# Kernel optimization log

Hardware: AMD Instinct MI355X
Metric: run time of the kernel (lower is better)

## Reference

```python
import jax, jax.numpy as jnp
import numpy as np

N_NODES = 10000
N_EDGES = 640000
D_IN, D_HID, D_OUT = 128, 256, 64


def setup_inputs() -> dict:
    key = jax.random.key(0)
    k = jax.random.split(key, 8)
    h = jax.random.normal(k[0], (N_NODES, D_IN), dtype=jnp.float32)
    w = jax.random.uniform(k[1], (N_EDGES, 1), dtype=jnp.float32)
    src = jax.random.randint(k[2], (N_EDGES,), 0, N_NODES, dtype=jnp.int32)
    dst = jax.random.randint(k[3], (N_EDGES,), 0, N_NODES, dtype=jnp.int32)
    W1 = jax.random.normal(k[4], (2 * D_IN, D_HID), dtype=jnp.float32) * (1.0 / np.sqrt(2 * D_IN))
    b1 = jnp.zeros((D_HID,), dtype=jnp.float32)
    W2 = jax.random.normal(k[5], (2 * D_HID, D_OUT), dtype=jnp.float32) * (1.0 / np.sqrt(2 * D_HID))
    b2 = jnp.zeros((D_OUT,), dtype=jnp.float32)
    return {"h": h, "w": w, "src": src, "dst": dst, "W1": W1, "b1": b1, "W2": W2, "b2": b2}


def _sage_layer(h, w, src, dst, W, b, n_nodes):
    # message: m_e = h[src_e] * w_e  (scalar edge weight broadcast over features)
    m = h[src] * w  # [E, D]
    # mean scatter-reduce over incoming edges per destination node
    s = jax.ops.segment_sum(m, dst, num_segments=n_nodes)          # [N, D]
    deg = jax.ops.segment_sum(jnp.ones((dst.shape[0],), h.dtype), dst, num_segments=n_nodes)
    h_N = jnp.where(deg[:, None] > 0, s / jnp.maximum(deg, 1.0)[:, None], 0.0)
    # concat + linear
    return jnp.concatenate([h, h_N], axis=1) @ W + b


def reference(h, w, src, dst, W1, b1, W2, b2):
    n = h.shape[0]
    x = _sage_layer(h, w, src, dst, W1, b1, n)
    x = jax.nn.relu(x)
    return _sage_layer(x, w, src, dst, W2, b2, n)
```

## Files before the change

kernel.cpp:

```cpp
#include <hip/hip_runtime.h>
#include <hip/hip_fp16.h>


#define NSUB 4
#define CAPS 64

typedef _Float16 f16x8 __attribute__((ext_vector_type(8)));
typedef float f32x4 __attribute__((ext_vector_type(4)));


__global__ __launch_bounds__(256) void prep_k(const float* __restrict__ h,
                                              const float* __restrict__ W1,
                                              const float* __restrict__ W2,
                                              int* __restrict__ cursor,
                                              __half* __restrict__ hh,
                                              __half* __restrict__ W1z,
                                              __half* __restrict__ W2z,
                                              int NC, int NH4) {
  const int t = blockIdx.x * blockDim.x + threadIdx.x;
  if (t < NC) {
    cursor[t] = 0;
    return;
  }
  const int tc = t - NC;
  if (tc < NH4) {
    const float4 v = reinterpret_cast<const float4*>(h)[tc];
    reinterpret_cast<__half2*>(hh)[2 * tc] = __floats2half2_rn(v.x, v.y);
    reinterpret_cast<__half2*>(hh)[2 * tc + 1] = __floats2half2_rn(v.z, v.w);
    return;
  }
  const int tw1 = tc - NH4;
  if (tw1 < 8192) {
    const int ln = tw1 & 63;
    const int nt = (tw1 >> 6) & 15;
    const int kc = tw1 >> 10;
    const int kbase = kc * 32 + (ln >> 4) * 8;
    const int n = nt * 16 + (ln & 15);
    __half tmp[8];
#pragma unroll
    for (int j = 0; j < 8; ++j)
      tmp[j] = __float2half_rn(W1[(size_t)(kbase + j) * 256 + n]);
    *reinterpret_cast<uint4*>(W1z + (size_t)tw1 * 8) = *reinterpret_cast<uint4*>(tmp);
    return;
  }
  const int tw2 = tw1 - 8192;
  if (tw2 < 4096) {
    const int ln = tw2 & 63;
    const int nt = (tw2 >> 6) & 7;
    const int kc = tw2 >> 9;
    const int kbase = kc * 32 + (ln >> 4) * 8;
    const int np = nt * 16 + (ln & 15);
    __half tmp[8];
#pragma unroll
    for (int j = 0; j < 8; ++j) {
      const int k = kbase + j;
      const float v = (np < 64) ? W2[(size_t)k * 64 + np]
                                : W2[(size_t)(256 + k) * 64 + (np - 64)];
      tmp[j] = __float2half_rn(v);
    }
    *reinterpret_cast<uint4*>(W2z + (size_t)tw2 * 8) = *reinterpret_cast<uint4*>(tmp);
  }
}


__global__ __launch_bounds__(256) void fill_k(const int* __restrict__ src,
                                              const int* __restrict__ dst,
                                              const float* __restrict__ w,
                                              int* __restrict__ cursor,
                                              unsigned int* __restrict__ ebuf,
                                              int E, int N) {
  const int grp = blockIdx.x & 7;
  const int bi = blockIdx.x >> 3;
  const int nbg = gridDim.x >> 3;
  const int chunk = (N + 7) >> 3;
  const int lo = grp * chunk;
  const int hi = min(N, lo + chunk);
  for (int i = bi * 256 + threadIdx.x; i < E; i += nbg * 256) {
    const int d = dst[i];
    if (d >= lo && d < hi) {
      const int sub = i & (NSUB - 1);
      const int p = atomicAdd(&cursor[d * NSUB + sub], 1);
      if (p < CAPS) {
        const __half hw = __float2half_rn(w[i]);
        ebuf[((size_t)(d * NSUB + sub)) * CAPS + p] =
            ((unsigned int)src[i] << 16) | (unsigned int)__half_as_ushort(hw);
      }
    }
  }
}

#define ACC8(q, wt)                                              \
  {                                                              \
    const float2 t0 = __half22float2(*(const __half2*)&(q).x);   \
    const float2 t1 = __half22float2(*(const __half2*)&(q).y);   \
    const float2 t2 = __half22float2(*(const __half2*)&(q).z);   \
    const float2 t3 = __half22float2(*(const __half2*)&(q).w);   \
    a[0] += t0.x * (wt); a[1] += t0.y * (wt);                    \
    a[2] += t1.x * (wt); a[3] += t1.y * (wt);                    \
    a[4] += t2.x * (wt); a[5] += t2.y * (wt);                    \
    a[6] += t3.x * (wt); a[7] += t3.y * (wt);                    \
  }


__global__ __launch_bounds__(256) void agg1_k(const __half* __restrict__ hh,
                                              const unsigned int* __restrict__ ebuf,
                                              const int* __restrict__ cnt,
                                              __half* __restrict__ G1, int N) {
  const int n = blockIdx.x * 4 + (threadIdx.x >> 6);
  if (n >= N) return;
  const int lane = threadIdx.x & 63;
  const int g = lane >> 4;
  const int f = lane & 15;
  const uint4* __restrict__ H = reinterpret_cast<const uint4*>(hh);
  float a[8] = {};
  int deg = 0;
#pragma unroll
  for (int seg = 0; seg < NSUB; ++seg) {
    const int m = min(cnt[n * NSUB + seg], CAPS);
    deg += m;
    const unsigned int* __restrict__ bkt = ebuf + ((size_t)(n * NSUB + seg)) * CAPS;
    const unsigned int pk = (lane < m) ? bkt[lane] : 0u;
    int j = 0;
    for (; j + 7 < m; j += 8) {
      const unsigned int pA = __shfl(pk, j + g);
      const unsigned int pB = __shfl(pk, j + 4 + g);
      const int eA = (int)(pA >> 16), eB = (int)(pB >> 16);
      const float wA = __half2float(__ushort_as_half((unsigned short)pA));
      const float wB = __half2float(__ushort_as_half((unsigned short)pB));
      const uint4 qA = H[(size_t)eA * 16 + f];
      const uint4 qB = H[(size_t)eB * 16 + f];
      ACC8(qA, wA)
      ACC8(qB, wB)
    }
    for (; j < m; j += 4) {
      const int jj = j + g;
      const unsigned int p = __shfl(pk, jj < m ? jj : (m - 1));
      float wt = __half2float(__ushort_as_half((unsigned short)p));
      if (jj >= m) wt = 0.f;
      const uint4 q = H[(size_t)(p >> 16) * 16 + f];
      ACC8(q, wt)
    }
  }
#pragma unroll
  for (int r = 0; r < 8; ++r) {
    a[r] += __shfl_xor(a[r], 16);
    a[r] += __shfl_xor(a[r], 32);
  }
  if (lane < 16) {
    const float inv = (deg > 0) ? 1.0f / (float)deg : 0.0f;
    __half tmp[8];
#pragma unroll
    for (int r = 0; r < 8; ++r) tmp[r] = __float2half_rn(a[r] * inv);
    reinterpret_cast<uint4*>(G1)[(size_t)n * 16 + f] = *reinterpret_cast<uint4*>(tmp);
  }
}


__global__ __launch_bounds__(256) void gemm1zu_k(const __half* __restrict__ hh,
                                                 const __half* __restrict__ G1,
                                                 const __half* __restrict__ W1z,
                                                 const float* __restrict__ b1,
                                                 const __half* __restrict__ W2z,
                                                 __half* __restrict__ Z,
                                                 float* __restrict__ U) {
  const int tid = threadIdx.x;
  const int w = tid >> 6, lane = tid & 63;
  const int m0 = blockIdx.x * 16;
  const int row_in = m0 + (lane & 15);
  const int qoff = (lane >> 4) * 8;
  const int colq = lane & 15;
  const int rowq = (lane >> 4) * 4;

  f32x4 acc[4] = {};
  const __half* __restrict__ Ah = hh + (size_t)row_in * 128;
  const __half* __restrict__ Ag = G1 + (size_t)row_in * 128;
#pragma unroll
  for (int kc = 0; kc < 8; ++kc) {
    const __half* asrc = (kc < 4) ? (Ah + kc * 32 + qoff) : (Ag + (kc - 4) * 32 + qoff);
    const f16x8 af = *reinterpret_cast<const f16x8*>(asrc);
    const __half* bbase = W1z + ((size_t)(kc * 16 + w * 4) * 64 + lane) * 8;
#pragma unroll
    for (int nt = 0; nt < 4; ++nt) {
      const f16x8 bf = *reinterpret_cast<const f16x8*>(bbase + (size_t)nt * 64 * 8);
      acc[nt] = __builtin_amdgcn_mfma_f32_16x16x32_f16(af, bf, acc[nt], 0, 0, 0);
    }
  }
  __shared__ alignas(16) __half Hs[16][264];
#pragma unroll
  for (int nt = 0; nt < 4; ++nt) {
    const int col = w * 64 + nt * 16 + colq;
    const float bz = b1[col];
#pragma unroll
    for (int r = 0; r < 4; ++r)
      Hs[rowq + r][col] = __float2half_rn(fmaxf(acc[nt][r] + bz, 0.f));
  }
  __syncthreads();

  f32x4 accz[2] = {};
#pragma unroll
  for (int kc = 0; kc < 8; ++kc) {
    const f16x8 af = *reinterpret_cast<const f16x8*>(&Hs[lane & 15][kc * 32 + qoff]);
    const __half* bbase = W2z + ((size_t)(kc * 8 + w * 2) * 64 + lane) * 8;
#pragma unroll
    for (int nt = 0; nt < 2; ++nt) {
      const f16x8 bf = *reinterpret_cast<const f16x8*>(bbase + (size_t)nt * 64 * 8);
      accz[nt] = __builtin_amdgcn_mfma_f32_16x16x32_f16(af, bf, accz[nt], 0, 0, 0);
    }
  }
  __shared__ float S[16][132];
#pragma unroll
  for (int nt = 0; nt < 2; ++nt) {
    const int col = w * 32 + nt * 16 + colq;
#pragma unroll
    for (int r = 0; r < 4; ++r) S[rowq + r][col] = accz[nt][r];
  }
  __syncthreads();
  {
    const int row = tid >> 4, c4 = tid & 15;
    const float4 v = make_float4(S[row][c4 * 4], S[row][c4 * 4 + 1],
                                 S[row][c4 * 4 + 2], S[row][c4 * 4 + 3]);
    *reinterpret_cast<float4*>(&U[(size_t)(m0 + row) * 64 + c4 * 4]) = v;
  }
  if (tid < 128) {
    const int row = tid >> 3, c8 = tid & 7;
    const float* s = &S[row][64 + c8 * 8];
    const __half2 h0 = __floats2half2_rn(s[0], s[1]);
    const __half2 h1 = __floats2half2_rn(s[2], s[3]);
    const __half2 h2 = __floats2half2_rn(s[4], s[5]);
    const __half2 h3 = __floats2half2_rn(s[6], s[7]);
    uint4 q;
    q.x = *reinterpret_cast<const unsigned int*>(&h0);
    q.y = *reinterpret_cast<const unsigned int*>(&h1);
    q.z = *reinterpret_cast<const unsigned int*>(&h2);
    q.w = *reinterpret_cast<const unsigned int*>(&h3);
    *reinterpret_cast<uint4*>(&Z[(size_t)(m0 + row) * 64 + c8 * 8]) = q;
  }
}


__global__ __launch_bounds__(256) void agg2z_k(const __half* __restrict__ Z,
                                               const float* __restrict__ U,
                                               const float* __restrict__ b2,
                                               const unsigned int* __restrict__ ebuf,
                                               const int* __restrict__ cnt,
                                               float* __restrict__ out, int N) {
  const int n = blockIdx.x * 4 + (threadIdx.x >> 6);
  if (n >= N) return;
  const int lane = threadIdx.x & 63;
  const int g = lane >> 3;
  const int f = lane & 7;
  const uint4* __restrict__ Zr = reinterpret_cast<const uint4*>(Z);
  float a[8] = {};
  int deg = 0;
#pragma unroll
  for (int seg = 0; seg < NSUB; ++seg) {
    const int m = min(cnt[n * NSUB + seg], CAPS);
    deg += m;
    const unsigned int* __restrict__ bkt = ebuf + ((size_t)(n * NSUB + seg)) * CAPS;
    const unsigned int pk = (lane < m) ? bkt[lane] : 0u;
    int j = 0;
    for (; j + 15 < m; j += 16) {
      const unsigned int pA = __shfl(pk, j + g);
      const unsigned int pB = __shfl(pk, j + 8 + g);
      const int eA = (int)(pA >> 16), eB = (int)(pB >> 16);
      const float wA = __half2float(__ushort_as_half((unsigned short)pA));
      const float wB = __half2float(__ushort_as_half((unsigned short)pB));
      const uint4 qA = Zr[(size_t)eA * 8 + f];
      const uint4 qB = Zr[(size_t)eB * 8 + f];
      ACC8(qA, wA)
      ACC8(qB, wB)
    }
    for (; j < m; j += 8) {
      const int jj = j + g;
      const unsigned int p = __shfl(pk, jj < m ? jj : (m - 1));
      float wt = __half2float(__ushort_as_half((unsigned short)p));
      if (jj >= m) wt = 0.f;
      const uint4 q = Zr[(size_t)(p >> 16) * 8 + f];
      ACC8(q, wt)
    }
  }
#pragma unroll
  for (int r = 0; r < 8; ++r) {
    a[r] += __shfl_xor(a[r], 8);
    a[r] += __shfl_xor(a[r], 16);
    a[r] += __shfl_xor(a[r], 32);
  }
  if (lane < 8) {
    const float inv = (deg > 0) ? 1.0f / (float)deg : 0.0f;
    const float4 u0 = *reinterpret_cast<const float4*>(&U[(size_t)n * 64 + f * 8]);
    const float4 u1 = *reinterpret_cast<const float4*>(&U[(size_t)n * 64 + f * 8 + 4]);
    const float4 z0 = *reinterpret_cast<const float4*>(&b2[f * 8]);
    const float4 z1 = *reinterpret_cast<const float4*>(&b2[f * 8 + 4]);
    float4 o0, o1;
    o0.x = a[0] * inv + u0.x + z0.x;
    o0.y = a[1] * inv + u0.y + z0.y;
    o0.z = a[2] * inv + u0.z + z0.z;
    o0.w = a[3] * inv + u0.w + z0.w;
    o1.x = a[4] * inv + u1.x + z1.x;
    o1.y = a[5] * inv + u1.y + z1.y;
    o1.z = a[6] * inv + u1.z + z1.z;
    o1.w = a[7] * inv + u1.w + z1.w;
    *reinterpret_cast<float4*>(&out[(size_t)n * 64 + f * 8]) = o0;
    *reinterpret_cast<float4*>(&out[(size_t)n * 64 + f * 8 + 4]) = o1;
  }
}


extern "C" void kernel_launch(void* const* d_in, const int* in_sizes, int n_in,
                              void* d_out, int out_size, void* d_ws, size_t ws_size,
                              hipStream_t stream) {
  const float* h   = (const float*)d_in[0];
  const float* w   = (const float*)d_in[1];
  const int*   src = (const int*)d_in[2];
  const int*   dst = (const int*)d_in[3];
  const float* W1  = (const float*)d_in[4];
  const float* b1  = (const float*)d_in[5];
  const float* W2  = (const float*)d_in[6];
  const float* b2  = (const float*)d_in[7];
  float* out = (float*)d_out;

  const int N = in_sizes[0] / 128;
  const int E = in_sizes[2];

  char* ws = (char*)d_ws;
  size_t o = 0;
  auto alloc = [&](size_t bytes) -> void* {
    void* p = ws + o;
    o = (o + bytes + 255) & ~(size_t)255;
    return p;
  };
  int*          cursor = (int*)alloc((size_t)N * NSUB * 4);
  unsigned int* ebuf   = (unsigned int*)alloc((size_t)N * NSUB * CAPS * 4);
  __half*       hh     = (__half*)alloc((size_t)N * 128 * 2);
  __half*       G1     = (__half*)alloc((size_t)N * 128 * 2);
  __half*       Z      = (__half*)alloc((size_t)N * 64 * 2);
  float*        U      = (float*)alloc((size_t)N * 64 * 4);
  __half*       W1z    = (__half*)alloc((size_t)256 * 256 * 2);
  __half*       W2z    = (__half*)alloc((size_t)256 * 128 * 2);

  const int NC = N * NSUB;
  const int NH4 = N * 32;
  const int prep_threads = NC + NH4 + 8192 + 4096;
  prep_k<<<(prep_threads + 255) / 256, 256, 0, stream>>>(h, W1, W2, cursor, hh,
                                                         W1z, W2z, NC, NH4);
  fill_k<<<2048, 256, 0, stream>>>(src, dst, w, cursor, ebuf, E, N);
  agg1_k<<<(N + 3) / 4, 256, 0, stream>>>(hh, ebuf, cursor, G1, N);
  gemm1zu_k<<<N / 16, 256, 0, stream>>>(hh, G1, W1z, b1, W2z, Z, U);
  agg2z_k<<<(N + 3) / 4, 256, 0, stream>>>(Z, U, b2, ebuf, cursor, out, N);
}
```

Baseline: 144.2 us.

## Merge prep into fill kernel, split node aggregation across two waves, remap blocks

Zeroing the cursors moves to a memset, and the h/weight fp16 conversion is folded into the fill kernel as extra blocks, which removes a launch. agg1 now splits each node's four sub-buckets across two waves and combines the partial sums through shared memory. agg1 and agg2 remap blocks so neighbouring block IDs touch the same destination-node chunk as fill_k's grouping. The intent is more parallelism per node and fewer launches, in exchange for an extra __syncthreads and shared-memory traffic.

```diff
diff --git a/kernel.cpp b/kernel.cpp
--- a/kernel.cpp
+++ b/kernel.cpp
@@ -9,27 +9,49 @@
 typedef float f32x4 __attribute__((ext_vector_type(4)));
 
 
-__global__ __launch_bounds__(256) void prep_k(const float* __restrict__ h,
+#define FB 2048
+
+__global__ __launch_bounds__(256) void fill_k(const int* __restrict__ src,
+                                              const int* __restrict__ dst,
+                                              const float* __restrict__ w,
+                                              const float* __restrict__ h,
                                               const float* __restrict__ W1,
                                               const float* __restrict__ W2,
                                               int* __restrict__ cursor,
+                                              unsigned int* __restrict__ ebuf,
                                               __half* __restrict__ hh,
                                               __half* __restrict__ W1z,
                                               __half* __restrict__ W2z,
-                                              int NC, int NH4) {
-  const int t = blockIdx.x * blockDim.x + threadIdx.x;
-  if (t < NC) {
-    cursor[t] = 0;
+                                              int E, int N, int NH4) {
+  if (blockIdx.x < FB) {
+    const int grp = blockIdx.x & 7;
+    const int bi = blockIdx.x >> 3;
+    const int nbg = FB >> 3;
+    const int chunk = (N + 7) >> 3;
+    const int lo = grp * chunk;
+    const int hi = min(N, lo + chunk);
+    for (int i = bi * 256 + threadIdx.x; i < E; i += nbg * 256) {
+      const int d = dst[i];
+      if (d >= lo && d < hi) {
+        const int sub = i & (NSUB - 1);
+        const int p = atomicAdd(&cursor[d * NSUB + sub], 1);
+        if (p < CAPS) {
+          const __half hw = __float2half_rn(w[i]);
+          ebuf[((size_t)(d * NSUB + sub)) * CAPS + p] =
+              ((unsigned int)src[i] << 16) | (unsigned int)__half_as_ushort(hw);
+        }
+      }
+    }
     return;
   }
-  const int tc = t - NC;
-  if (tc < NH4) {
-    const float4 v = reinterpret_cast<const float4*>(h)[tc];
-    reinterpret_cast<__half2*>(hh)[2 * tc] = __floats2half2_rn(v.x, v.y);
-    reinterpret_cast<__half2*>(hh)[2 * tc + 1] = __floats2half2_rn(v.z, v.w);
+  const int t = (blockIdx.x - FB) * 256 + threadIdx.x;
+  if (t < NH4) {
+    const float4 v = reinterpret_cast<const float4*>(h)[t];
+    reinterpret_cast<__half2*>(hh)[2 * t] = __floats2half2_rn(v.x, v.y);
+    reinterpret_cast<__half2*>(hh)[2 * t + 1] = __floats2half2_rn(v.z, v.w);
     return;
   }
-  const int tw1 = tc - NH4;
+  const int tw1 = t - NH4;
   if (tw1 < 8192) {
     const int ln = tw1 & 63;
     const int nt = (tw1 >> 6) & 15;
@@ -59,33 +81,6 @@
       tmp[j] = __float2half_rn(v);
     }
     *reinterpret_cast<uint4*>(W2z + (size_t)tw2 * 8) = *reinterpret_cast<uint4*>(tmp);
-  }
-}
-
-
-__global__ __launch_bounds__(256) void fill_k(const int* __restrict__ src,
-                                              const int* __restrict__ dst,
-                                              const float* __restrict__ w,
-                                              int* __restrict__ cursor,
-                                              unsigned int* __restrict__ ebuf,
-                                              int E, int N) {
-  const int grp = blockIdx.x & 7;
-  const int bi = blockIdx.x >> 3;
-  const int nbg = gridDim.x >> 3;
-  const int chunk = (N + 7) >> 3;
-  const int lo = grp * chunk;
-  const int hi = min(N, lo + chunk);
-  for (int i = bi * 256 + threadIdx.x; i < E; i += nbg * 256) {
-    const int d = dst[i];
-    if (d >= lo && d < hi) {
-      const int sub = i & (NSUB - 1);
-      const int p = atomicAdd(&cursor[d * NSUB + sub], 1);
-      if (p < CAPS) {
-        const __half hw = __float2half_rn(w[i]);
-        ebuf[((size_t)(d * NSUB + sub)) * CAPS + p] =
-            ((unsigned int)src[i] << 16) | (unsigned int)__half_as_ushort(hw);
-      }
-    }
   }
 }
 
@@ -106,39 +101,51 @@
                                               const unsigned int* __restrict__ ebuf,
                                               const int* __restrict__ cnt,
                                               __half* __restrict__ G1, int N) {
-  const int n = blockIdx.x * 4 + (threadIdx.x >> 6);
-  if (n >= N) return;
+  const int chunk = (N + 7) >> 3;
+  const int g8 = blockIdx.x & 7;
+  const int k = blockIdx.x >> 3;
+  const int wv = threadIdx.x >> 6;
+  const int node_sel = wv >> 1;
+  const int half = wv & 1;
+  const int loc = k * 2 + node_sel;
+  const int n = g8 * chunk + loc;
   const int lane = threadIdx.x & 63;
   const int g = lane >> 4;
   const int f = lane & 15;
   const uint4* __restrict__ H = reinterpret_cast<const uint4*>(hh);
+  __shared__ float part[2][2][16][8];
+  __shared__ int degs[2][2];
   float a[8] = {};
   int deg = 0;
-#pragma unroll
-  for (int seg = 0; seg < NSUB; ++seg) {
-    const int m = min(cnt[n * NSUB + seg], CAPS);
-    deg += m;
-    const unsigned int* __restrict__ bkt = ebuf + ((size_t)(n * NSUB + seg)) * CAPS;
-    const unsigned int pk = (lane < m) ? bkt[lane] : 0u;
-    int j = 0;
-    for (; j + 7 < m; j += 8) {
-      const unsigned int pA = __shfl(pk, j + g);
-      const unsigned int pB = __shfl(pk, j + 4 + g);
-      const int eA = (int)(pA >> 16), eB = (int)(pB >> 16);
-      const float wA = __half2float(__ushort_as_half((unsigned short)pA));
-      const float wB = __half2float(__ushort_as_half((unsigned short)pB));
-      const uint4 qA = H[(size_t)eA * 16 + f];
-      const uint4 qB = H[(size_t)eB * 16 + f];
-      ACC8(qA, wA)
-      ACC8(qB, wB)
-    }
-    for (; j < m; j += 4) {
-      const int jj = j + g;
-      const unsigned int p = __shfl(pk, jj < m ? jj : (m - 1));
-      float wt = __half2float(__ushort_as_half((unsigned short)p));
-      if (jj >= m) wt = 0.f;
-      const uint4 q = H[(size_t)(p >> 16) * 16 + f];
-      ACC8(q, wt)
+  const bool valid = (loc < chunk) && (n < N);
+  if (valid) {
+#pragma unroll
+    for (int s = 0; s < 2; ++s) {
+      const int seg = half * 2 + s;
+      const int m = min(cnt[n * NSUB + seg], CAPS);
+      deg += m;
+      const unsigned int* __restrict__ bkt =
+          ebuf + ((size_t)(n * NSUB + seg)) * CAPS;
+      const unsigned int pk = (lane < m) ? bkt[lane] : 0u;
+      int j = 0;
+      for (; j + 7 < m; j += 8) {
+        const unsigned int pA = __shfl(pk, j + g);
+        const unsigned int pB = __shfl(pk, j + 4 + g);
+        const float wA = __half2float(__ushort_as_half((unsigned short)pA));
+        const float wB = __half2float(__ushort_as_half((unsigned short)pB));
+        const uint4 qA = H[(size_t)(pA >> 16) * 16 + f];
+        const uint4 qB = H[(size_t)(pB >> 16) * 16 + f];
+        ACC8(qA, wA)
+        ACC8(qB, wB)
+      }
+      for (; j < m; j += 4) {
+        const int jj = j + g;
+        const unsigned int p = __shfl(pk, jj < m ? jj : (m - 1));
+        float wt = __half2float(__ushort_as_half((unsigned short)p));
+        if (jj >= m) wt = 0.f;
+        const uint4 q = H[(size_t)(p >> 16) * 16 + f];
+        ACC8(q, wt)
+      }
     }
   }
 #pragma unroll
@@ -147,10 +154,18 @@
     a[r] += __shfl_xor(a[r], 32);
   }
   if (lane < 16) {
-    const float inv = (deg > 0) ? 1.0f / (float)deg : 0.0f;
+#pragma unroll
+    for (int r = 0; r < 8; ++r) part[node_sel][half][f][r] = a[r];
+    if (f == 0) degs[node_sel][half] = deg;
+  }
+  __syncthreads();
+  if (half == 0 && lane < 16 && valid) {
+    const int d = degs[node_sel][0] + degs[node_sel][1];
+    const float inv = (d > 0) ? 1.0f / (float)d : 0.0f;
     __half tmp[8];
 #pragma unroll
-    for (int r = 0; r < 8; ++r) tmp[r] = __float2half_rn(a[r] * inv);
+    for (int r = 0; r < 8; ++r)
+      tmp[r] = __float2half_rn((part[node_sel][0][f][r] + part[node_sel][1][f][r]) * inv);
     reinterpret_cast<uint4*>(G1)[(size_t)n * 16 + f] = *reinterpret_cast<uint4*>(tmp);
   }
 }
@@ -244,8 +259,12 @@
                                                const unsigned int* __restrict__ ebuf,
                                                const int* __restrict__ cnt,
                                                float* __restrict__ out, int N) {
-  const int n = blockIdx.x * 4 + (threadIdx.x >> 6);
-  if (n >= N) return;
+  const int chunk = (N + 7) >> 3;
+  const int g8 = blockIdx.x & 7;
+  const int k = blockIdx.x >> 3;
+  const int loc = k * 4 + (threadIdx.x >> 6);
+  const int n = g8 * chunk + loc;
+  if (loc >= chunk || n >= N) return;
   const int lane = threadIdx.x & 63;
   const int g = lane >> 3;
   const int f = lane & 7;
@@ -262,11 +281,10 @@
     for (; j + 15 < m; j += 16) {
       const unsigned int pA = __shfl(pk, j + g);
       const unsigned int pB = __shfl(pk, j + 8 + g);
-      const int eA = (int)(pA >> 16), eB = (int)(pB >> 16);
       const float wA = __half2float(__ushort_as_half((unsigned short)pA));
       const float wB = __half2float(__ushort_as_half((unsigned short)pB));
-      const uint4 qA = Zr[(size_t)eA * 8 + f];
-      const uint4 qB = Zr[(size_t)eB * 8 + f];
+      const uint4 qA = Zr[(size_t)(pA >> 16) * 8 + f];
+      const uint4 qB = Zr[(size_t)(pB >> 16) * 8 + f];
       ACC8(qA, wA)
       ACC8(qB, wB)
     }
@@ -338,13 +356,14 @@
   __half*       W1z    = (__half*)alloc((size_t)256 * 256 * 2);
   __half*       W2z    = (__half*)alloc((size_t)256 * 128 * 2);
 
-  const int NC = N * NSUB;
   const int NH4 = N * 32;
-  const int prep_threads = NC + NH4 + 8192 + 4096;
-  prep_k<<<(prep_threads + 255) / 256, 256, 0, stream>>>(h, W1, W2, cursor, hh,
-                                                         W1z, W2z, NC, NH4);
-  fill_k<<<2048, 256, 0, stream>>>(src, dst, w, cursor, ebuf, E, N);
-  agg1_k<<<(N + 3) / 4, 256, 0, stream>>>(hh, ebuf, cursor, G1, N);
+  const int prep_blocks = (NH4 + 8192 + 4096 + 255) / 256;
+  const int chunk = (N + 7) >> 3;
+
+  hipMemsetAsync(cursor, 0, (size_t)N * NSUB * 4, stream);
+  fill_k<<<FB + prep_blocks, 256, 0, stream>>>(src, dst, w, h, W1, W2, cursor,
+                                               ebuf, hh, W1z, W2z, E, N, NH4);
+  agg1_k<<<8 * ((chunk + 1) / 2), 256, 0, stream>>>(hh, ebuf, cursor, G1, N);
   gemm1zu_k<<<N / 16, 256, 0, stream>>>(hh, G1, W1z, b1, W2z, Z, U);
-  agg2z_k<<<(N + 3) / 4, 256, 0, stream>>>(Z, U, b2, ebuf, cursor, out, N);
-}
+  agg2z_k<<<8 * ((chunk + 3) / 4), 256, 0, stream>>>(Z, U, b2, ebuf, cursor, out, N);
+}
```

Result: no change. 143.6 us (median of 2 runs) (-0.4%).
